# Kernel tuning notes

Hardware: AMD Instinct MI355X
Metric: run time of the kernel (lower is better)

## Reference

```python
import jax, jax.numpy as jnp
import numpy as np

N_NODES = 100000
N_EDGES = 1600000
N_GRAPHS = 512


def gcn_conv(x, row, col, W, b):
    # x: [N, Cin], row/col: [E] (self-loops already appended)
    n = x.shape[0]
    h = x @ W                                        # [N, Cout]
    deg = jax.ops.segment_sum(jnp.ones_like(col, dtype=x.dtype), col, num_segments=n)
    dinv = jnp.where(deg > 0, deg ** -0.5, 0.0)
    norm = dinv[row] * dinv[col]                     # [E]
    msg = norm[:, None] * h[row]                     # [E, Cout]
    out = jax.ops.segment_sum(msg, col, num_segments=n)
    return out + b


def setup_inputs() -> dict:
    key = jax.random.key(0)
    ks = jax.random.split(key, 10)
    x = jax.random.normal(ks[0], (N_NODES, 128), dtype=jnp.float32)
    edge_index = jax.random.randint(ks[1], (2, N_EDGES), 0, N_NODES, dtype=jnp.int64)
    batch = jnp.sort(jax.random.randint(ks[2], (N_NODES,), 0, N_GRAPHS, dtype=jnp.int64))
    def lin_w(k, fan_in, fan_out):
        bound = 1.0 / np.sqrt(fan_in)
        return jax.random.uniform(k, (fan_in, fan_out), jnp.float32, -bound, bound)
    # GCN layers (bias zero-initialized per reset_parameters)
    W1 = lin_w(ks[3], 128, 128); b1 = jnp.zeros((128,), jnp.float32)
    W2 = lin_w(ks[4], 128, 128); b2 = jnp.zeros((128,), jnp.float32)
    # MLP layers (Linear with bias)
    Wm1 = lin_w(ks[5], 128, 64)
    bm1 = jax.random.uniform(ks[6], (64,), jnp.float32, -1/np.sqrt(128), 1/np.sqrt(128))
    Wm2 = lin_w(ks[7], 64, 1)
    bm2 = jax.random.uniform(ks[8], (1,), jnp.float32, -1/np.sqrt(64), 1/np.sqrt(64))
    return {"x": x, "edge_index": edge_index, "batch": batch,
            "W1": W1, "b1": b1, "W2": W2, "b2": b2,
            "Wm1": Wm1, "bm1": bm1, "Wm2": Wm2, "bm2": bm2}


def reference(x, edge_index, batch, W1, b1, W2, b2, Wm1, bm1, Wm2, bm2):
    n = x.shape[0]
    loops = jnp.arange(n, dtype=edge_index.dtype)
    row = jnp.concatenate([edge_index[0], loops])
    col = jnp.concatenate([edge_index[1], loops])
    # GCN: conv -> relu -> conv
    h = gcn_conv(x, row, col, W1, b1)
    h = jax.nn.relu(h)
    h = gcn_conv(h, row, col, W2, b2)
    # scatter-mean pooling over graphs
    sums = jax.ops.segment_sum(h, batch, num_segments=N_GRAPHS)      # [G, C]
    counts = jax.ops.segment_sum(jnp.ones((n,), h.dtype), batch, num_segments=N_GRAPHS)
    g = sums / jnp.maximum(counts, 1.0)[:, None]
    # MLP: linear -> relu -> linear
    g = jax.nn.relu(g @ Wm1 + bm1)
    out = g @ Wm2 + bm2
    return out
```

## Files before the change

kernel.cpp:

```cpp
#include <hip/hip_runtime.h>
#include <math.h>

#define C_DIM 128
#define POOL_CHUNK 64
#define BKT_SHIFT 7
#define MAX_B 1024
#define CB 256
#define CHUNK_MAX 6400
#define FB_CAP 8192
typedef unsigned short ushort_t;
typedef __attribute__((ext_vector_type(8))) short short8;
typedef __attribute__((ext_vector_type(4))) float f32x4;
typedef __attribute__((ext_vector_type(2))) float f32x2;

static inline int ceil_div(int a, int b) { return (a + b - 1) / b; }

__device__ inline ushort_t f2bf(float f) {
    union { float f; unsigned u; } v; v.f = f;
    unsigned r = v.u + 0x7FFFu + ((v.u >> 16) & 1u);
    return (ushort_t)(r >> 16);
}
__device__ inline float bf_lo(unsigned u) {
    union { unsigned v; float f; } c; c.v = u << 16; return c.f;
}
__device__ inline float bf_hi(unsigned u) {
    union { unsigned v; float f; } c; c.v = u & 0xFFFF0000u; return c.f;
}
__device__ inline void accum8pk(uint4 u, f32x2 ac[4]) {
    ac[0] += (f32x2){bf_lo(u.x), bf_hi(u.x)};
    ac[1] += (f32x2){bf_lo(u.y), bf_hi(u.y)};
    ac[2] += (f32x2){bf_lo(u.z), bf_hi(u.z)};
    ac[3] += (f32x2){bf_lo(u.w), bf_hi(u.w)};
}

__global__ __launch_bounds__(512) void k_sortchunk(
    const int* __restrict__ row, const int* __restrict__ col, int E, int chunk,
    int B, int* __restrict__ counts, int* __restrict__ sstart,
    int* __restrict__ epk,
    const float* __restrict__ W1, const float* __restrict__ W2,
    uint4* __restrict__ wf1, uint4* __restrict__ wf2,
    float* __restrict__ gsums, int GC, int* __restrict__ cursor) {
    int t = threadIdx.x, blk = blockIdx.x;
    if (blk >= CB) {
        const float* W = (blk == CB) ? W1 : W2;
        uint4* wf = (blk == CB) ? wf1 : wf2;
        for (int f = t; f < 2048; f += 512) {
            int lane = f & 63, kkn = f >> 6;
            int kk = kkn & 3, nt = kkn >> 2;
            int n = lane & 15, quad = lane >> 4;
            union { ushort_t h[8]; uint4 v; } u;
#pragma unroll
            for (int j = 0; j < 8; ++j)
                u.h[j] = f2bf(W[(size_t)(kk * 32 + quad * 8 + j) * C_DIM + nt * 16 + n]);
            wf[f] = u.v;
        }
        return;
    }
    for (int i = blk * 512 + t; i < GC; i += CB * 512) gsums[i] = 0.f;
    if (blk == 0 && t == 0) *cursor = 0;

    __shared__ int hist[MAX_B];
    __shared__ int hscan[MAX_B];
    __shared__ int sd[512];
    __shared__ __align__(16) int ebuf[CHUNK_MAX];
    __shared__ __align__(8)  ushort_t bbuf[CHUNK_MAX];
    __shared__ int sorted[CHUNK_MAX];

    for (int i = t; i < B; i += 512) hist[i] = 0;
    __syncthreads();
    int s = blk * chunk;
    int e = s + chunk; if (e > E) e = E;
    int cnt = e - s;
    for (int i = s + 4 * t; i < e; i += 2048) {
        int4 c = *(const int4*)(col + i);
        int4 r = *(const int4*)(row + i);
        int li = i - s;
        int4 pk;
        pk.x = (r.x << 7) | (c.x & 127);
        pk.y = (r.y << 7) | (c.y & 127);
        pk.z = (r.z << 7) | (c.z & 127);
        pk.w = (r.w << 7) | (c.w & 127);
        *(int4*)&ebuf[li] = pk;
        ushort4 bk;
        bk.x = (ushort_t)(c.x >> BKT_SHIFT);
        bk.y = (ushort_t)(c.y >> BKT_SHIFT);
        bk.z = (ushort_t)(c.z >> BKT_SHIFT);
        bk.w = (ushort_t)(c.w >> BKT_SHIFT);
        *(ushort4*)&bbuf[li] = bk;
        atomicAdd(&hist[bk.x], 1);
        atomicAdd(&hist[bk.y], 1);
        atomicAdd(&hist[bk.z], 1);
        atomicAdd(&hist[bk.w], 1);
    }
    __syncthreads();
    {
        int base2 = t * 2;
        int vv[2]; int sum = 0;
#pragma unroll
        for (int j = 0; j < 2; ++j) {
            int idx = base2 + j;
            vv[j] = (idx < B) ? hist[idx] : 0;
            sum += vv[j];
        }
        sd[t] = sum;
        __syncthreads();
        for (int off = 1; off < 512; off <<= 1) {
            int x = (t >= off) ? sd[t - off] : 0;
            __syncthreads();
            sd[t] += x;
            __syncthreads();
        }
        int run = sd[t] - sum;
#pragma unroll
        for (int j = 0; j < 2; ++j) {
            int idx = base2 + j;
            if (idx < B) hscan[idx] = run;
            run += vv[j];
        }
    }
    __syncthreads();
    for (int i = t; i < B; i += 512) {
        counts[(size_t)blk * MAX_B + i] = hist[i];
        sstart[(size_t)blk * MAX_B + i] = hscan[i];
    }
    __syncthreads();
    for (int i = t; i < B; i += 512) hist[i] = hscan[i];
    __syncthreads();
    for (int i = t; i < cnt; i += 512) {
        int pos = atomicAdd(&hist[bbuf[i]], 1);
        sorted[pos] = ebuf[i];
    }
    __syncthreads();
    for (int i = t; i * 4 < cnt; i += 512)
        *(int4*)&epk[s + i * 4] = *(const int4*)&sorted[i * 4];
}

__global__ __launch_bounds__(256) void k_bfinal(
    const int* __restrict__ epk, const int* __restrict__ counts,
    const int* __restrict__ sstart, int* __restrict__ cursor,
    int chunk, int N,
    int2* __restrict__ offs2, float* __restrict__ dinv, int* __restrict__ csr) {
    __shared__ int sh[FB_CAP];
    __shared__ int sd[256];
    __shared__ int cnt[128];
    __shared__ int pre[128];
    __shared__ int cur[128];
    __shared__ int sbase_s;
    int bkt = blockIdx.x, t = threadIdx.x;
    int base = bkt << BKT_SHIFT;
    int nn = N - base; if (nn > 128) nn = 128;

    int segln = counts[(size_t)t * MAX_B + bkt];
    int gs = t * chunk + sstart[(size_t)t * MAX_B + bkt];
    sd[t] = segln;
    __syncthreads();
    for (int off = 1; off < 256; off <<= 1) {
        int x = (t >= off) ? sd[t - off] : 0;
        __syncthreads();
        sd[t] += x;
        __syncthreads();
    }
    int place = sd[t] - segln;
    int m = sd[255];
    if (t == 255) sbase_s = atomicAdd(cursor, m);
    if (t < 128) cnt[t] = 0;
    __syncthreads();
    int sbase = sbase_s;

    bool fits = (m <= FB_CAP);
    if (fits) {
        for (int j = 0; j < segln; ++j) {
            int u = epk[gs + j];
            sh[place + j] = u;
            atomicAdd(&cnt[u & 127], 1);
        }
    } else {
        for (int j = 0; j < segln; ++j)
            atomicAdd(&cnt[epk[gs + j] & 127], 1);
    }
    __syncthreads();
    if (t < 128) pre[t] = cnt[t];
    __syncthreads();
    for (int off = 1; off < 128; off <<= 1) {
        int x = (t >= off && t < 128) ? pre[t - off] : 0;
        __syncthreads();
        if (t < 128) pre[t] += x;
        __syncthreads();
    }
    if (t < 128) {
        int ex = pre[t] - cnt[t];
        cur[t] = ex;
        if (t < nn) {
            offs2[base + t] = make_int2(sbase + ex, sbase + ex + cnt[t]);
            dinv[base + t] = 1.0f / sqrtf((float)cnt[t] + 1.0f);
        }
    }
    __syncthreads();
    if (fits) {
        for (int i = t; i < m; i += 256) {
            int u = sh[i];
            int slot = atomicAdd(&cur[u & 127], 1);
            csr[sbase + slot] = (u >> 7) << 8;
        }
    } else {
        for (int j = 0; j < segln; ++j) {
            int u = epk[gs + j];
            int slot = atomicAdd(&cur[u & 127], 1);
            csr[sbase + slot] = (u >> 7) << 8;
        }
    }
}

template <int ABF16>
__global__ __launch_bounds__(256) void k_matmul_mfma(
    const float* __restrict__ Af, const ushort_t* __restrict__ Abf,
    const uint4* __restrict__ wfrag, const float* __restrict__ dinv,
    ushort_t* __restrict__ Cb, int N) {
    __shared__ uint4 wfs[2048];
    __shared__ __align__(16) ushort_t As[64 * 136];
    int t = threadIdx.x;
    int wv = t >> 6, lane = t & 63;
    int n = lane & 15, quad = lane >> 4;
    int row0 = blockIdx.x * 64;

    for (int i = t; i < 2048; i += 256) wfs[i] = wfrag[i];

    if (ABF16) {
#pragma unroll
        for (int i = 0; i < 4; ++i) {
            int idx = i * 256 + t;
            int r = idx >> 4, c8 = idx & 15;
            int grow = row0 + r; if (grow >= N) grow = N - 1;
            uint4 u = *(const uint4*)(Abf + (size_t)grow * C_DIM + c8 * 8);
            *(uint4*)&As[r * 136 + c8 * 8] = u;
        }
    } else {
#pragma unroll
        for (int i = 0; i < 8; ++i) {
            int idx = i * 256 + t;
            int r = idx >> 5, cq = idx & 31;
            int grow = row0 + r; if (grow >= N) grow = N - 1;
            float4 f = *(const float4*)(Af + (size_t)grow * C_DIM + cq * 4);
            union { ushort_t h[4]; uint2 v; } c;
            c.h[0] = f2bf(f.x); c.h[1] = f2bf(f.y);
            c.h[2] = f2bf(f.z); c.h[3] = f2bf(f.w);
            *(uint2*)&As[r * 136 + cq * 4] = c.v;
        }
    }

    f32x4 acc[8];
#pragma unroll
    for (int i = 0; i < 8; ++i) acc[i] = (f32x4){0.f, 0.f, 0.f, 0.f};

    __syncthreads();

    int rl = wv * 16 + n;
#pragma unroll
    for (int kk = 0; kk < 4; ++kk) {
        union { uint4 v; short8 s; } ca;
        ca.v = *(const uint4*)&As[rl * 136 + kk * 32 + quad * 8];
#pragma unroll
        for (int nt = 0; nt < 8; ++nt) {
            union { uint4 v; short8 s; } cb;
            cb.v = wfs[(nt * 4 + kk) * 64 + lane];
            acc[nt] = __builtin_amdgcn_mfma_f32_16x16x32_bf16(ca.s, cb.s, acc[nt], 0, 0, 0);
        }
    }

    __syncthreads();
#pragma unroll
    for (int reg = 0; reg < 4; ++reg) {
        int lr = wv * 16 + quad * 4 + reg;
        int grow = row0 + lr;
        float sc = dinv[grow < N ? grow : N - 1];
#pragma unroll
        for (int nt = 0; nt < 8; ++nt)
            As[lr * 136 + nt * 16 + n] = f2bf(acc[nt][reg] * sc);
    }
    __syncthreads();
    int rows = N - row0; if (rows > 64) rows = 64;
    for (int idx = t; idx < 16 * 64; idx += 256) {
        int r = idx >> 4, c8 = idx & 15;
        if (r < rows)
            *(uint4*)(Cb + (size_t)(row0 + r) * C_DIM + c8 * 8) =
                *(const uint4*)&As[r * 136 + c8 * 8];
    }
}

template <int RELU>
__global__ __launch_bounds__(256) void k_aggregate(
    const ushort_t* __restrict__ hs, const int2* __restrict__ offs2,
    const int* __restrict__ csr, const float* __restrict__ dinv,
    const float* __restrict__ bias, uint4* __restrict__ outV, int N) {
    int node = (blockIdx.x << 2) + (threadIdx.x >> 6);
    if (node >= N) return;
    int t = threadIdx.x & 63;
    int q = t >> 4;
    int fs = t & 15;
    const char* hb = (const char*)hs;
    unsigned fso = (unsigned)(fs * 16);
    int2 se = offs2[node];
    int s = se.x, e = se.y;

    f32x2 ac[4];
    {
        uint4 u = *(const uint4*)(hb + ((unsigned)node << 8) + fso);
        if (q == 0) {
            ac[0] = (f32x2){bf_lo(u.x), bf_hi(u.x)};
            ac[1] = (f32x2){bf_lo(u.y), bf_hi(u.y)};
            ac[2] = (f32x2){bf_lo(u.z), bf_hi(u.z)};
            ac[3] = (f32x2){bf_lo(u.w), bf_hi(u.w)};
        } else {
#pragma unroll
            for (int i = 0; i < 4; ++i) ac[i] = (f32x2){0.f, 0.f};
        }
    }

    int j = s;
    for (; j + 16 <= e; j += 16) {
        int r[4];
#pragma unroll
        for (int b = 0; b < 4; ++b)
            r[b] = __builtin_nontemporal_load(csr + j + b * 4 + q);
        uint4 u[4];
#pragma unroll
        for (int b = 0; b < 4; ++b)
            u[b] = *(const uint4*)(hb + (unsigned)r[b] + fso);
#pragma unroll
        for (int b = 0; b < 4; ++b) accum8pk(u[b], ac);
    }
    for (; j + 4 <= e; j += 4) {
        int r = __builtin_nontemporal_load(csr + j + q);
        uint4 u = *(const uint4*)(hb + (unsigned)r + fso);
        accum8pk(u, ac);
    }
    if (j + q < e) {
        int r = __builtin_nontemporal_load(csr + j + q);
        uint4 u = *(const uint4*)(hb + (unsigned)r + fso);
        accum8pk(u, ac);
    }

#pragma unroll
    for (int i = 0; i < 4; ++i) {
        ac[i].x += __shfl_xor(ac[i].x, 16);
        ac[i].y += __shfl_xor(ac[i].y, 16);
        ac[i].x += __shfl_xor(ac[i].x, 32);
        ac[i].y += __shfl_xor(ac[i].y, 32);
    }

    if (q == 0) {
        float dn = dinv[node];
        float4 b0 = *(const float4*)(bias + fs * 8);
        float4 b1 = *(const float4*)(bias + fs * 8 + 4);
        float o[8];
        o[0] = dn * ac[0].x + b0.x; o[1] = dn * ac[0].y + b0.y;
        o[2] = dn * ac[1].x + b0.z; o[3] = dn * ac[1].y + b0.w;
        o[4] = dn * ac[2].x + b1.x; o[5] = dn * ac[2].y + b1.y;
        o[6] = dn * ac[3].x + b1.z; o[7] = dn * ac[3].y + b1.w;
        if (RELU) {
#pragma unroll
            for (int i = 0; i < 8; ++i) o[i] = fmaxf(o[i], 0.f);
        }
        uint4 pk;
        pk.x = (unsigned)f2bf(o[0]) | ((unsigned)f2bf(o[1]) << 16);
        pk.y = (unsigned)f2bf(o[2]) | ((unsigned)f2bf(o[3]) << 16);
        pk.z = (unsigned)f2bf(o[4]) | ((unsigned)f2bf(o[5]) << 16);
        pk.w = (unsigned)f2bf(o[6]) | ((unsigned)f2bf(o[7]) << 16);
        outV[(size_t)node * 16 + fs] = pk;
    }
}

__global__ __launch_bounds__(128) void k_pool_sum(
    const ushort_t* __restrict__ h, const int* __restrict__ batch, int n,
    float* __restrict__ sums) {
    int r0 = blockIdx.x * POOL_CHUNK;
    int r1 = r0 + POOL_CHUNK; if (r1 > n) r1 = n;
    if (r0 >= n) return;
    int t = threadIdx.x;
    int c = t & 63, rr = t >> 6;
    float2 acc = make_float2(0.f, 0.f);
    int g = batch[r0];
    int i = r0;
    while (i < r1) {
        if (i + 8 <= r1 && batch[i + 7] == g) {
#pragma unroll
            for (int b = 0; b < 4; ++b) {
                unsigned u = *(const unsigned*)(h + (size_t)(i + rr + 2 * b) * C_DIM + c * 2);
                acc.x += bf_lo(u); acc.y += bf_hi(u);
            }
            i += 8;
        } else {
            int bi = batch[i];
            if (bi != g) {
                atomicAdd(&sums[(size_t)g * C_DIM + c * 2], acc.x);
                atomicAdd(&sums[(size_t)g * C_DIM + c * 2 + 1], acc.y);
                acc = make_float2(0.f, 0.f); g = bi;
            }
            if (rr == 0) {
                unsigned u = *(const unsigned*)(h + (size_t)i * C_DIM + c * 2);
                acc.x += bf_lo(u); acc.y += bf_hi(u);
            }
            ++i;
        }
    }
    atomicAdd(&sums[(size_t)g * C_DIM + c * 2], acc.x);
    atomicAdd(&sums[(size_t)g * C_DIM + c * 2 + 1], acc.y);
}

__global__ __launch_bounds__(128) void k_mlp(
    const float* __restrict__ sums, const int* __restrict__ batch, int n,
    const float* __restrict__ Wm1, const float* __restrict__ bm1,
    const float* __restrict__ Wm2, const float* __restrict__ bm2,
    float* __restrict__ out) {
    int g = blockIdx.x;
    int t = threadIdx.x;
    int lo = 0, hi = n;
    while (lo < hi) { int m = (lo + hi) >> 1; if (batch[m] < g) lo = m + 1; else hi = m; }
    int start = lo;
    lo = start; hi = n;
    while (lo < hi) { int m = (lo + hi) >> 1; if (batch[m] < g + 1) lo = m + 1; else hi = m; }
    float cnt = (float)(lo - start);

    float mean = sums[(size_t)g * C_DIM + t] / fmaxf(cnt, 1.0f);

    __shared__ float m_s[128];
    __shared__ float hid[64];
    m_s[t] = mean;
    __syncthreads();
    if (t < 64) {
        float a = bm1[t];
#pragma unroll 4
        for (int k = 0; k < 128; ++k) a += m_s[k] * Wm1[k * 64 + t];
        hid[t] = fmaxf(a, 0.f) * Wm2[t];
    }
    __syncthreads();
    if (t < 64) {
        float v = hid[t];
        for (int off = 32; off > 0; off >>= 1) v += __shfl_down(v, off);
        if (t == 0) out[g] = v + bm2[0];
    }
}

extern "C" void kernel_launch(void* const* d_in, const int* in_sizes, int n_in,
                              void* d_out, int out_size, void* d_ws, size_t ws_size,
                              hipStream_t stream) {
    const float* x     = (const float*)d_in[0];
    const int*   eidx  = (const int*)d_in[1];
    const int*   batch = (const int*)d_in[2];
    const float* W1    = (const float*)d_in[3];
    const float* b1    = (const float*)d_in[4];
    const float* W2    = (const float*)d_in[5];
    const float* b2    = (const float*)d_in[6];
    const float* Wm1   = (const float*)d_in[7];
    const float* bm1   = (const float*)d_in[8];
    const float* Wm2   = (const float*)d_in[9];
    const float* bm2   = (const float*)d_in[10];

    const int N = in_sizes[2];
    const int E = in_sizes[1] / 2;
    const int G = out_size;
    const int B = (N + 127) >> BKT_SHIFT;

    char* p = (char*)d_ws;
    auto carve = [&](size_t bytes) {
        char* q = p;
        p += (bytes + 255) & ~(size_t)255;
        return q;
    };
    ushort_t* bufT   = (ushort_t*)carve((size_t)N * C_DIM * sizeof(ushort_t));
    ushort_t* bufA   = (ushort_t*)carve((size_t)N * C_DIM * sizeof(ushort_t));
    float*    dinv   = (float*)   carve((size_t)N * sizeof(float));
    int2*     offs2  = (int2*)    carve((size_t)N * sizeof(int2));
    int*      csr    = (int*)     carve((size_t)E * sizeof(int));
    int*      counts = (int*)     carve((size_t)CB * MAX_B * sizeof(int));
    int*      sstart = (int*)     carve((size_t)CB * MAX_B * sizeof(int));
    float*    gsums  = (float*)   carve((size_t)G * C_DIM * sizeof(float));
    uint4*    wf1    = (uint4*)   carve(2048 * sizeof(uint4));
    uint4*    wf2    = (uint4*)   carve(2048 * sizeof(uint4));
    int*      cursor = (int*)     carve(sizeof(int));
    int*      epk    = (int*)bufT;

    const int* erow = eidx;
    const int* ecol = eidx + E;
    const int chunk = (ceil_div(E, CB) + 3) & ~3;

    k_sortchunk<<<CB + 2, 512, 0, stream>>>(erow, ecol, E, chunk, B,
                                            counts, sstart, epk,
                                            W1, W2, wf1, wf2, gsums, G * C_DIM, cursor);
    k_bfinal<<<B, 256, 0, stream>>>(epk, counts, sstart, cursor, chunk, N,
                                    offs2, dinv, csr);

    k_matmul_mfma<0><<<ceil_div(N, 64), 256, 0, stream>>>(x, nullptr, wf1, dinv, bufT, N);
    k_aggregate<1><<<ceil_div(N, 4), 256, 0, stream>>>(bufT, offs2, csr, dinv, b1,
                                                       (uint4*)bufA, N);
    k_matmul_mfma<1><<<ceil_div(N, 64), 256, 0, stream>>>(nullptr, bufA, wf2, dinv, bufT, N);
    k_aggregate<0><<<ceil_div(N, 4), 256, 0, stream>>>(bufT, offs2, csr, dinv, b2,
                                                       (uint4*)bufA, N);
    k_pool_sum<<<ceil_div(N, POOL_CHUNK), 128, 0, stream>>>(bufA, batch, N, gsums);
    k_mlp<<<G, 128, 0, stream>>>(gsums, batch, N, Wm1, bm1, Wm2, bm2, (float*)d_out);
}
```

Measured before the change: 324.9 us.

## Pad CSR rows to multiples of four and aggregate two nodes per wavefront

```diff
diff --git a/kernel.cpp b/kernel.cpp
--- a/kernel.cpp
+++ b/kernel.cpp
@@ -162,10 +162,8 @@
     }
     int place = sd[t] - segln;
     int m = sd[255];
-    if (t == 255) sbase_s = atomicAdd(cursor, m);
     if (t < 128) cnt[t] = 0;
     __syncthreads();
-    int sbase = sbase_s;
 
     bool fits = (m <= FB_CAP);
     if (fits) {
@@ -179,7 +177,7 @@
             atomicAdd(&cnt[epk[gs + j] & 127], 1);
     }
     __syncthreads();
-    if (t < 128) pre[t] = cnt[t];
+    if (t < 128) pre[t] = (cnt[t] + 3) & ~3;
     __syncthreads();
     for (int off = 1; off < 128; off <<= 1) {
         int x = (t >= off && t < 128) ? pre[t - off] : 0;
@@ -187,11 +185,15 @@
         if (t < 128) pre[t] += x;
         __syncthreads();
     }
+    if (t == 127) sbase_s = atomicAdd(cursor, pre[127]);
+    __syncthreads();
+    int sbase = sbase_s;
     if (t < 128) {
-        int ex = pre[t] - cnt[t];
+        int c4 = (cnt[t] + 3) & ~3;
+        int ex = pre[t] - c4;
         cur[t] = ex;
         if (t < nn) {
-            offs2[base + t] = make_int2(sbase + ex, sbase + ex + cnt[t]);
+            offs2[base + t] = make_int2(sbase + ex, sbase + ex + c4);
             dinv[base + t] = 1.0f / sqrtf((float)cnt[t] + 1.0f);
         }
     }
@@ -208,6 +210,13 @@
             int slot = atomicAdd(&cur[u & 127], 1);
             csr[sbase + slot] = (u >> 7) << 8;
         }
+    }
+    __syncthreads();
+    if (t < nn) {
+        int c4 = (cnt[t] + 3) & ~3;
+        int ex = pre[t] - c4;
+        int zoff = N << 8;
+        for (int k2 = cnt[t]; k2 < c4; ++k2) csr[sbase + ex + k2] = zoff;
     }
 }
 
@@ -284,6 +293,8 @@
         if (r < rows)
             *(uint4*)(Cb + (size_t)(row0 + r) * C_DIM + c8 * 8) =
                 *(const uint4*)&As[r * 136 + c8 * 8];
+        else if (row0 + r == N)
+            *(uint4*)(Cb + (size_t)N * C_DIM + c8 * 8) = (uint4){0, 0, 0, 0};
     }
 }
 
@@ -292,63 +303,71 @@
     const ushort_t* __restrict__ hs, const int2* __restrict__ offs2,
     const int* __restrict__ csr, const float* __restrict__ dinv,
     const float* __restrict__ bias, uint4* __restrict__ outV, int N) {
-    int node = (blockIdx.x << 2) + (threadIdx.x >> 6);
-    if (node >= N) return;
     int t = threadIdx.x & 63;
-    int q = t >> 4;
+    int half = t >> 5;
+    int q2 = (t >> 4) & 1;
     int fs = t & 15;
+    int node = (blockIdx.x << 3) + ((threadIdx.x >> 6) << 1) + half;
+    bool valid = node < N;
+    if (!valid) node = N - 1;
     const char* hb = (const char*)hs;
-    unsigned fso = (unsigned)(fs * 16);
+    unsigned fso = (unsigned)(fs << 4);
     int2 se = offs2[node];
-    int s = se.x, e = se.y;
+    int j = se.x, e = se.y;
 
     f32x2 ac[4];
-    {
+    if (q2 == 0) {
         uint4 u = *(const uint4*)(hb + ((unsigned)node << 8) + fso);
-        if (q == 0) {
-            ac[0] = (f32x2){bf_lo(u.x), bf_hi(u.x)};
-            ac[1] = (f32x2){bf_lo(u.y), bf_hi(u.y)};
-            ac[2] = (f32x2){bf_lo(u.z), bf_hi(u.z)};
-            ac[3] = (f32x2){bf_lo(u.w), bf_hi(u.w)};
-        } else {
-#pragma unroll
-            for (int i = 0; i < 4; ++i) ac[i] = (f32x2){0.f, 0.f};
-        }
-    }
-
-    int j = s;
+        ac[0] = (f32x2){bf_lo(u.x), bf_hi(u.x)};
+        ac[1] = (f32x2){bf_lo(u.y), bf_hi(u.y)};
+        ac[2] = (f32x2){bf_lo(u.z), bf_hi(u.z)};
+        ac[3] = (f32x2){bf_lo(u.w), bf_hi(u.w)};
+    } else {
+#pragma unroll
+        for (int i = 0; i < 4; ++i) ac[i] = (f32x2){0.f, 0.f};
+    }
+
     for (; j + 16 <= e; j += 16) {
-        int r[4];
-#pragma unroll
-        for (int b = 0; b < 4; ++b)
-            r[b] = __builtin_nontemporal_load(csr + j + b * 4 + q);
-        uint4 u[4];
-#pragma unroll
-        for (int b = 0; b < 4; ++b)
-            u[b] = *(const uint4*)(hb + (unsigned)r[b] + fso);
-#pragma unroll
-        for (int b = 0; b < 4; ++b) accum8pk(u[b], ac);
-    }
-    for (; j + 4 <= e; j += 4) {
-        int r = __builtin_nontemporal_load(csr + j + q);
-        uint4 u = *(const uint4*)(hb + (unsigned)r + fso);
-        accum8pk(u, ac);
-    }
-    if (j + q < e) {
-        int r = __builtin_nontemporal_load(csr + j + q);
-        uint4 u = *(const uint4*)(hb + (unsigned)r + fso);
-        accum8pk(u, ac);
+        const int4* cp = (const int4*)(csr + j + (q2 << 3));
+        int4 ra = cp[0];
+        int4 rb = cp[1];
+        uint4 u0 = *(const uint4*)(hb + (unsigned)ra.x + fso);
+        uint4 u1 = *(const uint4*)(hb + (unsigned)ra.y + fso);
+        uint4 u2 = *(const uint4*)(hb + (unsigned)ra.z + fso);
+        uint4 u3 = *(const uint4*)(hb + (unsigned)ra.w + fso);
+        uint4 u4 = *(const uint4*)(hb + (unsigned)rb.x + fso);
+        uint4 u5 = *(const uint4*)(hb + (unsigned)rb.y + fso);
+        uint4 u6 = *(const uint4*)(hb + (unsigned)rb.z + fso);
+        uint4 u7 = *(const uint4*)(hb + (unsigned)rb.w + fso);
+        accum8pk(u0, ac); accum8pk(u1, ac);
+        accum8pk(u2, ac); accum8pk(u3, ac);
+        accum8pk(u4, ac); accum8pk(u5, ac);
+        accum8pk(u6, ac); accum8pk(u7, ac);
+    }
+    if (j + 8 <= e) {
+        int4 ra = *(const int4*)(csr + j + (q2 << 2));
+        uint4 u0 = *(const uint4*)(hb + (unsigned)ra.x + fso);
+        uint4 u1 = *(const uint4*)(hb + (unsigned)ra.y + fso);
+        uint4 u2 = *(const uint4*)(hb + (unsigned)ra.z + fso);
+        uint4 u3 = *(const uint4*)(hb + (unsigned)ra.w + fso);
+        accum8pk(u0, ac); accum8pk(u1, ac);
+        accum8pk(u2, ac); accum8pk(u3, ac);
+        j += 8;
+    }
+    if (j + 4 <= e) {
+        int2 rc = *(const int2*)(csr + j + (q2 << 1));
+        uint4 u0 = *(const uint4*)(hb + (unsigned)rc.x + fso);
+        uint4 u1 = *(const uint4*)(hb + (unsigned)rc.y + fso);
+        accum8pk(u0, ac); accum8pk(u1, ac);
     }
 
 #pragma unroll
     for (int i = 0; i < 4; ++i) {
         ac[i].x += __shfl_xor(ac[i].x, 16);
         ac[i].y += __shfl_xor(ac[i].y, 16);
-        ac[i].x += __shfl_xor(ac[i].x, 32);
-        ac[i].y += __shfl_xor(ac[i].y, 32);
-    }
-
-    if (q == 0) {
+    }
+
+    if (q2 == 0 && valid) {
         float dn = dinv[node];
         float4 b0 = *(const float4*)(bias + fs * 8);
         float4 b1 = *(const float4*)(bias + fs * 8 + 4);
@@ -467,11 +486,11 @@
         p += (bytes + 255) & ~(size_t)255;
         return q;
     };
-    ushort_t* bufT   = (ushort_t*)carve((size_t)N * C_DIM * sizeof(ushort_t));
+    ushort_t* bufT   = (ushort_t*)carve((size_t)(N + 1) * C_DIM * sizeof(ushort_t));
     ushort_t* bufA   = (ushort_t*)carve((size_t)N * C_DIM * sizeof(ushort_t));
     float*    dinv   = (float*)   carve((size_t)N * sizeof(float));
     int2*     offs2  = (int2*)    carve((size_t)N * sizeof(int2));
-    int*      csr    = (int*)     carve((size_t)E * sizeof(int));
+    int*      csr    = (int*)     carve(((size_t)E + 3 * (size_t)N + 64) * sizeof(int));
     int*      counts = (int*)     carve((size_t)CB * MAX_B * sizeof(int));
     int*      sstart = (int*)     carve((size_t)CB * MAX_B * sizeof(int));
     float*    gsums  = (float*)   carve((size_t)G * C_DIM * sizeof(float));
@@ -491,10 +510,10 @@
                                     offs2, dinv, csr);
 
     k_matmul_mfma<0><<<ceil_div(N, 64), 256, 0, stream>>>(x, nullptr, wf1, dinv, bufT, N);
-    k_aggregate<1><<<ceil_div(N, 4), 256, 0, stream>>>(bufT, offs2, csr, dinv, b1,
+    k_aggregate<1><<<ceil_div(N, 8), 256, 0, stream>>>(bufT, offs2, csr, dinv, b1,
                                                        (uint4*)bufA, N);
     k_matmul_mfma<1><<<ceil_div(N, 64), 256, 0, stream>>>(nullptr, bufA, wf2, dinv, bufT, N);
-    k_aggregate<0><<<ceil_div(N, 4), 256, 0, stream>>>(bufT, offs2, csr, dinv, b2,
+    k_aggregate<0><<<ceil_div(N, 8), 256, 0, stream>>>(bufT, offs2, csr, dinv, b2,
                                                        (uint4*)bufA, N);
     k_pool_sum<<<ceil_div(N, POOL_CHUNK), 128, 0, stream>>>(bufA, batch, N, gsums);
     k_mlp<<<G, 128, 0, stream>>>(gsums, batch, N, Wm1, bm1, Wm2, bm2, (float*)d_out);
```

Measured after the change: 306.6 us. -5.6%, faster.
